# Performance work log

Measured on AMD Instinct MI355X. Metric: run time of the kernel, lower is better.

## Reference

```python
import jax, jax.numpy as jnp
import numpy as np
from jax import lax


def setup_inputs() -> dict:
    key = jax.random.key(0)
    ks = jax.random.split(key, 6)
    B, C, H, W = 8, 128, 64, 64   # C = 2*channel, channel (per-branch) c = 64
    c = C // 2
    return {
        "x_up": jax.random.normal(ks[0], (B, C, H, W), dtype=jnp.float32),
        "x_skip": jax.random.normal(ks[1], (B, C, H, W), dtype=jnp.float32),
        # nn.Linear(c, 2c): weight [out,in], bias [out]
        "kv1_w": jax.random.normal(ks[2], (2 * c, c), dtype=jnp.float32) * 0.05,
        "kv1_b": jnp.zeros((2 * c,), dtype=jnp.float32),
        "kv2_w": jax.random.normal(ks[3], (2 * c, c), dtype=jnp.float32) * 0.05,
        "kv2_b": jnp.zeros((2 * c,), dtype=jnp.float32),
        # Conv2d(2c, 2c, 3, stride 1, pad 1, bias=False), OIHW
        "conv_w": jax.random.normal(ks[4], (C, C, 3, 3), dtype=jnp.float32) * 0.05,
        # BatchNorm2d(2c) in inference form (running stats)
        "bn_gamma": jax.random.normal(ks[5], (C,), dtype=jnp.float32) * 0.1 + 1.0,
        "bn_beta": jnp.zeros((C,), dtype=jnp.float32),
        "bn_mean": jnp.zeros((C,), dtype=jnp.float32),
        "bn_var": jnp.ones((C,), dtype=jnp.float32),
    }


def reference(x_up, x_skip, kv1_w, kv1_b, kv2_w, kv2_b, conv_w,
              bn_gamma, bn_beta, bn_mean, bn_var):
    b, C, h, w = x_up.shape
    c = C // 2
    hw = h * w
    up1, up2 = x_up[:, :c], x_up[:, c:]
    sk1, sk2 = x_skip[:, :c], x_skip[:, c:]

    # ---- spatial attention branch (softmax over last axis, hw x hw) ----
    shortcut1 = up1 + sk1
    u1 = up1.reshape(b, c, hw).transpose(0, 2, 1)   # (b, hw, c)
    s1 = sk1.reshape(b, c, hw).transpose(0, 2, 1)   # (b, hw, c)
    kv = s1 @ kv1_w.T + kv1_b                        # (b, hw, 2c)
    k1, v1 = kv[..., :c], kv[..., c:]
    attn = jax.nn.softmax(jnp.einsum('bnc,bmc->bnm', u1, k1), axis=-1)  # (b, hw, hw)
    sout = jnp.einsum('bnm,bmc->bnc', attn, v1)      # (b, hw, c)
    sout = sout.transpose(0, 2, 1).reshape(b, c, h, w) + shortcut1

    # ---- channel attention branch (softmax over dim=1 of the c x c map) ----
    shortcut2 = up2 + sk2
    u2 = up2.reshape(b, c, hw).transpose(0, 2, 1)    # (b, hw, c)
    s2 = sk2.reshape(b, c, hw).transpose(0, 2, 1)
    kv = s2 @ kv2_w.T + kv2_b                        # (b, hw, 2c)
    k2, v2 = kv[..., :c], kv[..., c:]
    A = jax.nn.softmax(jnp.einsum('bnc,bnd->bcd', u2, k2), axis=1)  # (b, c, c)
    cout = jnp.einsum('bnc,bcd->bnd', v2, A)          # (b, hw, c)
    cout = cout.transpose(0, 2, 1).reshape(b, c, h, w) + shortcut2

    # ---- conv + BN (inference) + ReLU ----
    x = jnp.concatenate([sout, cout], axis=1)         # (b, 2c, h, w)
    y = lax.conv_general_dilated(x, conv_w, (1, 1), 'SAME',
                                 dimension_numbers=('NCHW', 'OIHW', 'NCHW'))
    inv = jax.lax.rsqrt(bn_var + 1e-5)
    y = (y - bn_mean[None, :, None, None]) * (inv * bn_gamma)[None, :, None, None] \
        + bn_beta[None, :, None, None]
    return jax.nn.relu(y)
```

## Files before the change

kernel.cpp:

```cpp
#include <hip/hip_runtime.h>
#include <math.h>

#define HW 4096

typedef __attribute__((ext_vector_type(8))) short bh8;
typedef __attribute__((ext_vector_type(4))) float f32x4;
typedef __attribute__((ext_vector_type(2))) unsigned int u32x2;
typedef unsigned int u32;
typedef unsigned short u16;

__device__ __forceinline__ u16 f2bf(float f) {
  union { float f; u32 u; } v; v.f = f;
  u32 u = v.u;
  return (u16)((u + 0x7FFFu + ((u >> 16) & 1u)) >> 16);
}
__device__ __forceinline__ float bf2f(u16 h) {
  union { u32 u; float f; } v; v.u = ((u32)h) << 16;
  return v.f;
}
__device__ __forceinline__ u32 cvt_pk_bf16(float lo, float hi) {
  u32 r;
  asm("v_cvt_pk_bf16_f32 %0, %1, %2" : "=v"(r) : "v"(lo), "v"(hi));
  return r;
}
__device__ __forceinline__ float fexp2(float x) {
  float r;
  asm("v_exp_f32 %0, %1" : "=v"(r) : "v"(x));
  return r;
}

__global__ __launch_bounds__(256) void kv_proj(
    const float* __restrict__ xs,
    const float* __restrict__ w1, const float* __restrict__ b1,
    const float* __restrict__ w2, const float* __restrict__ b2,
    u32* __restrict__ Knm, u16* __restrict__ Vcm,
    u16* __restrict__ K2t, u16* __restrict__ V2t,
    const float* __restrict__ cw, const float* __restrict__ gamma,
    const float* __restrict__ beta, const float* __restrict__ mean,
    const float* __restrict__ var, u16* __restrict__ Wg,
    float* __restrict__ shb) {
  __shared__ float Ss[64][65];
  __shared__ float Ws[128 * 64];
  __shared__ u32 LtK[64][33];
  const int b = blockIdx.y, n0 = blockIdx.x * 64;
  const int t = threadIdx.x;
  const int lane_n = t & 63, jg = t >> 6;
  const int jbase = jg * 32;
  const float* xsb = xs + (size_t)b * 128 * HW;

  {
    int gid = (blockIdx.y * 64 + blockIdx.x) * 256 + t;
    for (int i = gid; i < 147456; i += 131072) {
      int tap = i >> 14, oc = (i >> 7) & 127, ic = i & 127;
      float sc = gamma[oc] * rsqrtf(var[oc] + 1e-5f);
      Wg[i] = f2bf(cw[((size_t)(oc * 128 + ic)) * 9 + tap] * sc);
    }
    if (gid < 128) {
      float sc = gamma[gid] * rsqrtf(var[gid] + 1e-5f);
      shb[gid] = beta[gid] - mean[gid] * sc;
    }
  }

  for (int br = 0; br < 2; ++br) {
    const float* W = br ? w2 : w1;
    const float* bias = br ? b2 : b1;
    const float* src = xsb + (br ? 64 * HW : 0);
    __syncthreads();
    for (int s = 0; s < 16; ++s) {
      int ch = s * 4 + jg;
      Ss[ch][lane_n] = src[(size_t)ch * HW + n0 + lane_n];
    }
    for (int i = t; i < 128 * 64; i += 256) Ws[i] = W[i];
    __syncthreads();

    float acc[32];
#pragma unroll
    for (int i = 0; i < 32; ++i) acc[i] = bias[jbase + i];
    for (int ch = 0; ch < 64; ++ch) {
      float s = Ss[ch][lane_n];
#pragma unroll
      for (int i = 0; i < 32; ++i) acc[i] = fmaf(Ws[(jbase + i) * 64 + ch], s, acc[i]);
    }

    if (br == 0) {
      if (jg < 2) {
#pragma unroll
        for (int i2 = 0; i2 < 16; ++i2) {
          u32 p = (u32)f2bf(acc[2 * i2]) | ((u32)f2bf(acc[2 * i2 + 1]) << 16);
          LtK[lane_n][jg * 16 + i2] = p;
        }
      } else {
#pragma unroll
        for (int i = 0; i < 32; ++i) {
          int ch = jbase - 64 + i;
          Vcm[((size_t)b * 64 + ch) * HW + n0 + lane_n] = f2bf(acc[i]);
        }
      }
      __syncthreads();
#pragma unroll
      for (int p = 0; p < 8; ++p) {
        int idx = p * 256 + t;
        int n = idx >> 5, cc = idx & 31;
        Knm[((size_t)b * HW + n0 + n) * 32 + cc] = LtK[n][cc];
      }
    } else {
      u16* Kt = K2t + (size_t)b * 64 * HW;
      u16* Vt = V2t + (size_t)b * 64 * HW;
#pragma unroll
      for (int i = 0; i < 32; ++i) {
        int j = jbase + i;
        u16* dst = (j < 64) ? (Kt + (size_t)j * HW) : (Vt + (size_t)(j - 64) * HW);
        dst[n0 + lane_n] = f2bf(acc[i]);
      }
    }
  }
}

__device__ __forceinline__ void attn_step(
    const bh8* kf, const bh8* vf, const bh8 (&qb)[4][2], const bh8 ones,
    f32x4 (&O)[4][4], f32x4 (&Osum)[4]) {
  f32x4 S[2][4];
  __builtin_amdgcn_s_setprio(1);
#pragma unroll
  for (int mt = 0; mt < 2; ++mt)
#pragma unroll
    for (int nt = 0; nt < 4; ++nt) {
      f32x4 a = (f32x4)(0.f);
      a = __builtin_amdgcn_mfma_f32_16x16x32_bf16(kf[mt * 2 + 0], qb[nt][0], a, 0, 0, 0);
      a = __builtin_amdgcn_mfma_f32_16x16x32_bf16(kf[mt * 2 + 1], qb[nt][1], a, 0, 0, 0);
      S[mt][nt] = a;
    }
  __builtin_amdgcn_s_setprio(0);
#pragma unroll
  for (int nt = 0; nt < 4; ++nt) {
    const float c = 17.312340f;
    float e00 = fexp2(S[0][nt][0] - c), e01 = fexp2(S[0][nt][1] - c);
    float e02 = fexp2(S[0][nt][2] - c), e03 = fexp2(S[0][nt][3] - c);
    float e10 = fexp2(S[1][nt][0] - c), e11 = fexp2(S[1][nt][1] - c);
    float e12 = fexp2(S[1][nt][2] - c), e13 = fexp2(S[1][nt][3] - c);
    u32 A = cvt_pk_bf16(e00, e01);
    u32 B = cvt_pk_bf16(e02, e03);
    u32 C = cvt_pk_bf16(e10, e11);
    u32 D = cvt_pk_bf16(e12, e13);
    u32x2 rac = __builtin_amdgcn_permlane32_swap(A, C, 0, 0);
    u32x2 rbd = __builtin_amdgcn_permlane32_swap(B, D, 0, 0);
    u32x2 r02 = __builtin_amdgcn_permlane16_swap(rac.x, rac.y, 0, 0);
    u32x2 r13 = __builtin_amdgcn_permlane16_swap(rbd.x, rbd.y, 0, 0);
    union { u32 u[4]; bh8 v; } pb;
    pb.u[0] = r02.x;
    pb.u[1] = r13.x;
    pb.u[2] = r02.y;
    pb.u[3] = r13.y;
    __builtin_amdgcn_s_setprio(1);
#pragma unroll
    for (int ct = 0; ct < 4; ++ct)
      O[ct][nt] = __builtin_amdgcn_mfma_f32_16x16x32_bf16(vf[ct], pb.v, O[ct][nt], 0, 0, 0);
    Osum[nt] = __builtin_amdgcn_mfma_f32_16x16x32_bf16(ones, pb.v, Osum[nt], 0, 0, 0);
    __builtin_amdgcn_s_setprio(0);
  }
}

#define LOADKV(KB, KF, VF)                                            \
  do {                                                                \
    const int n0_ = (KB) * 128;                                       \
    const u16* kr_ = Kb + (size_t)(n0_ + wb + lq) * 64 + quad * 8;    \
    KF[0] = *(const bh8*)(kr_);                                       \
    KF[1] = *(const bh8*)(kr_ + 32);                                  \
    KF[2] = *(const bh8*)(kr_ + 1024);                                \
    KF[3] = *(const bh8*)(kr_ + 1056);                                \
    const u16* vr_ = Vb + (size_t)lq * HW + n0_ + wb + quad * 8;      \
    VF[0] = *(const bh8*)(vr_);                                       \
    VF[1] = *(const bh8*)(vr_ + 16 * HW);                             \
    VF[2] = *(const bh8*)(vr_ + 32 * HW);                             \
    VF[3] = *(const bh8*)(vr_ + 48 * HW);                             \
  } while (0)

__global__ __launch_bounds__(256, 2) void attn_gram(
    const float* __restrict__ xu, const float* __restrict__ xs,
    const u16* __restrict__ Knm, const u16* __restrict__ Vcm,
    u16* __restrict__ xcat,
    const u16* __restrict__ K2t, float* __restrict__ Mp) {
  __shared__ __align__(16) u16 SMEM[18432];
  const int b = blockIdx.y;
  const int t = threadIdx.x;

  if (blockIdx.x >= 64) {
    float* Us = (float*)SMEM;
    float* Ksm = Us + 64 * 65;
    const int n0 = (blockIdx.x - 64) * 128;
    const int c = t & 63, dg = t >> 6;
    const float* ub = xu + ((size_t)b * 128 + 64) * HW;
    const u16* kb2 = K2t + (size_t)b * 64 * HW;
    float acc[16];
#pragma unroll
    for (int i = 0; i < 16; ++i) acc[i] = 0.f;
    for (int s = 0; s < 2; ++s) {
      int nn = n0 + s * 64;
      __syncthreads();
      for (int r = 0; r < 16; ++r) {
        int row = r * 4 + dg;
        Us[row * 65 + c] = ub[(size_t)row * HW + nn + c];
        Ksm[row * 65 + c] = bf2f(kb2[(size_t)row * HW + nn + c]);
      }
      __syncthreads();
      for (int n = 0; n < 64; ++n) {
        float u = Us[c * 65 + n];
#pragma unroll
        for (int i = 0; i < 16; ++i)
          acc[i] = fmaf(Ksm[(dg * 16 + i) * 65 + n], u, acc[i]);
      }
    }
    float* dst = Mp + ((size_t)(blockIdx.x - 64) * 8 + b) * 4096 + c * 64 + dg * 16;
#pragma unroll
    for (int i = 0; i < 16; ++i) dst[i] = acc[i];
    return;
  }

  const int q0 = blockIdx.x * 64;
  const int wq = t >> 6, lane = t & 63, lq = lane & 15, quad = lane >> 4;
  const int wb = wq * 32;
  const float* xub = xu + (size_t)b * 128 * HW;
  const float* xsb = xs + (size_t)b * 128 * HW;
  const u16* Kb = Knm + (size_t)b * HW * 64;
  const u16* Vb = Vcm + (size_t)b * 64 * HW;

  bh8 qb[4][2];
#pragma unroll
  for (int nt = 0; nt < 4; ++nt)
#pragma unroll
    for (int s = 0; s < 2; ++s)
#pragma unroll
      for (int j = 0; j < 8; ++j) {
        int ch = s * 32 + quad * 8 + j;
        qb[nt][s][j] =
            (short)f2bf(xub[(size_t)ch * HW + q0 + nt * 16 + lq] * 1.44269504f);
      }
  bh8 ones;
#pragma unroll
  for (int j = 0; j < 8; ++j) ones[j] = (short)0x3F80;

  f32x4 O[4][4];
#pragma unroll
  for (int ct = 0; ct < 4; ++ct)
#pragma unroll
    for (int nt = 0; nt < 4; ++nt) O[ct][nt] = (f32x4)(0.f);
  f32x4 Osum[4];
#pragma unroll
  for (int nt = 0; nt < 4; ++nt) Osum[nt] = (f32x4)(0.f);

  bh8 kfa[4], vfa[4], kfb[4], vfb[4];
  LOADKV(0, kfa, vfa);
  for (int kb = 0; kb < 32; kb += 2) {
    LOADKV(kb + 1, kfb, vfb);
    attn_step(kfa, vfa, qb, ones, O, Osum);
    if (kb + 2 < 32) LOADKV(kb + 2, kfa, vfa);
    attn_step(kfb, vfb, qb, ones, O, Osum);
  }

  float* Posc = (float*)SMEM;
  float* Lred = (float*)(SMEM + 17408);
  if (quad == 0) {
#pragma unroll
    for (int nt = 0; nt < 4; ++nt) Lred[(wq * 4 + nt) * 16 + lq] = Osum[nt][0];
  }

  const int q = t & 63, cg = t >> 6;
#pragma unroll
  for (int rh = 0; rh < 2; ++rh) {
    if (rh) __syncthreads();
#pragma unroll
    for (int c2 = 0; c2 < 2; ++c2)
#pragma unroll
      for (int nt = 0; nt < 4; ++nt)
#pragma unroll
        for (int r = 0; r < 4; ++r)
          Posc[(wq * 32 + c2 * 16 + quad * 4 + r) * 68 + nt * 16 + lq] =
              O[rh * 2 + c2][nt][r];
    __syncthreads();
    float li = 0.f;
#pragma unroll
    for (int w2 = 0; w2 < 4; ++w2) li += Lred[w2 * 64 + q];
    float inv = 1.f / li;
    u16 h[8];
#pragma unroll
    for (int i = 0; i < 8; ++i) {
      int chl = cg * 8 + i;
      float s = 0.f;
#pragma unroll
      for (int w2 = 0; w2 < 4; ++w2) s += Posc[(w2 * 32 + chl) * 68 + q];
      int ch = rh * 32 + chl;
      size_t g = (size_t)ch * HW + q0 + q;
      h[i] = f2bf(s * inv + xub[g] + xsb[g]);
    }
    u32 pk[4];
#pragma unroll
    for (int j = 0; j < 4; ++j) pk[j] = (u32)h[2 * j] | ((u32)h[2 * j + 1] << 16);
    u16* ob = xcat + ((size_t)b * HW + q0 + q) * 128 + rh * 32 + cg * 8;
    *(uint4*)ob = make_uint4(pk[0], pk[1], pk[2], pk[3]);
  }
}

__global__ void chan_reduce(const float* __restrict__ Mp, float* __restrict__ M) {
  int idx = blockIdx.x * 256 + threadIdx.x;
  float s = 0.f;
  for (int ch = 0; ch < 32; ++ch) s += Mp[(size_t)ch * 32768 + idx];
  M[idx] = s;
}

__global__ __launch_bounds__(256) void chan_apply(
    const u16* __restrict__ V2t, const float* __restrict__ M,
    const float* __restrict__ xu, const float* __restrict__ xs,
    u16* __restrict__ xcat) {
  __shared__ float Vsm[64][65];
  __shared__ float As[64][65];
  __shared__ float red1[4][64], red2[4][64];
  const int b = blockIdx.y, n0 = blockIdx.x * 64, t = threadIdx.x;
  const int lane = t & 63, dg = t >> 6;
  const u16* Vb = V2t + (size_t)b * 64 * HW;
  for (int s = 0; s < 16; ++s) {
    int c = s * 4 + dg;
    Vsm[lane][c] = bf2f(Vb[(size_t)c * HW + n0 + lane]);
  }
  for (int idx = t; idx < 4096; idx += 256) As[idx >> 6][idx & 63] = M[b * 4096 + idx];
  __syncthreads();
  float mx = -1e30f;
#pragma unroll
  for (int i = 0; i < 16; ++i) mx = fmaxf(mx, As[dg * 16 + i][lane]);
  red1[dg][lane] = mx;
  __syncthreads();
  mx = fmaxf(fmaxf(red1[0][lane], red1[1][lane]), fmaxf(red1[2][lane], red1[3][lane]));
  float se = 0.f;
#pragma unroll
  for (int i = 0; i < 16; ++i) {
    float e = __expf(As[dg * 16 + i][lane] - mx);
    As[dg * 16 + i][lane] = e;
    se += e;
  }
  red2[dg][lane] = se;
  __syncthreads();

  float acc[16];
#pragma unroll
  for (int i = 0; i < 16; ++i) acc[i] = 0.f;
  for (int c = 0; c < 64; ++c) {
    float v = Vsm[lane][c];
#pragma unroll
    for (int i = 0; i < 16; ++i) acc[i] = fmaf(v, As[c][dg * 16 + i], acc[i]);
  }
  const float* xub = xu + ((size_t)b * 128 + 64) * HW;
  const float* xsb = xs + ((size_t)b * 128 + 64) * HW;
  const int n = n0 + lane;
  u16 hv[16];
#pragma unroll
  for (int i = 0; i < 16; ++i) {
    int d = dg * 16 + i;
    float sm = red2[0][d] + red2[1][d] + red2[2][d] + red2[3][d];
    hv[i] = f2bf(acc[i] / sm + xub[(size_t)d * HW + n] + xsb[(size_t)d * HW + n]);
  }
  u32 pk[8];
#pragma unroll
  for (int j = 0; j < 8; ++j) pk[j] = (u32)hv[2 * j] | ((u32)hv[2 * j + 1] << 16);
  u16* ob = xcat + ((size_t)b * HW + n) * 128 + 64 + dg * 16;
  *(uint4*)(ob) = make_uint4(pk[0], pk[1], pk[2], pk[3]);
  *(uint4*)(ob + 8) = make_uint4(pk[4], pk[5], pk[6], pk[7]);
}

__global__ __launch_bounds__(512) void conv_mfma(
    const u16* __restrict__ X, const u16* __restrict__ Wg,
    const float* __restrict__ shb, float* __restrict__ out) {
  __shared__ __align__(16) u16 In[4 * 66 * 136];
  __shared__ __align__(16) u16 Wt[2][128 * 136];
  const int b = blockIdx.y, h0 = blockIdx.x * 2;
  const int t = threadIdx.x;
  const int wq = t >> 6, lane = t & 63, lq = lane & 15, quad = lane >> 4;
  const int nb = (wq & 1) * 64;
  const int mb = (wq >> 1) * 2;
  const u16* Xb = X + (size_t)b * HW * 128;

  if (t < 128) {
    int ih = t >> 5, iwsel = (t >> 4) & 1, ck = t & 15;
    int iw = iwsel ? 65 : 0;
    *(uint4*)&In[(ih * 66 + iw) * 136 + ck * 8] = make_uint4(0, 0, 0, 0);
  }
  for (int ih = 0; ih < 4; ++ih) {
    int h = h0 - 1 + ih;
    bool ok = (h >= 0 && h < 64);
    const u16* src = Xb + (size_t)h * 64 * 128;
#pragma unroll
    for (int p = 0; p < 2; ++p) {
      int idx = p * 512 + t;
      int row = idx >> 4, ck = idx & 15;
      uint4 d = make_uint4(0, 0, 0, 0);
      if (ok) d = *(const uint4*)(src + (size_t)row * 128 + ck * 8);
      *(uint4*)&In[(ih * 66 + 1 + row) * 136 + ck * 8] = d;
    }
  }
  {
    const u16* src = Wg;
#pragma unroll
    for (int p = 0; p < 4; ++p) {
      int idx = p * 512 + t;
      int oc = idx >> 4, ck = idx & 15;
      uint4 d = *(const uint4*)(src + oc * 128 + ck * 8);
      *(uint4*)&Wt[0][oc * 136 + ck * 8] = d;
    }
  }
  __syncthreads();

  f32x4 acc[2][4];
#pragma unroll
  for (int mt = 0; mt < 2; ++mt)
#pragma unroll
    for (int nt = 0; nt < 4; ++nt) acc[mt][nt] = (f32x4)(0.f);

  for (int tap = 0; tap < 9; ++tap) {
    const int cur = tap & 1;
    if (tap < 8) {
      const u16* src = Wg + (size_t)(tap + 1) * 128 * 128;
#pragma unroll
      for (int p = 0; p < 4; ++p) {
        int idx = p * 512 + t;
        int oc = idx >> 4, ck = idx & 15;
        uint4 d = *(const uint4*)(src + oc * 128 + ck * 8);
        *(uint4*)&Wt[cur ^ 1][oc * 136 + ck * 8] = d;
      }
    }
    const int dh = tap / 3, dw = tap - 3 * dh;
    const u16* Wc = &Wt[cur][0];
#pragma unroll
    for (int c = 0; c < 4; ++c) {
      bh8 bf[4];
#pragma unroll
      for (int nt = 0; nt < 4; ++nt)
        bf[nt] = *(const bh8*)&Wc[(nb + nt * 16 + lq) * 136 + c * 32 + quad * 8];
#pragma unroll
      for (int mt = 0; mt < 2; ++mt) {
        int s = (mb + mt) * 16 + lq;
        int ih = (s >> 6) + dh, iw = (s & 63) + dw;
        bh8 af = *(const bh8*)&In[(ih * 66 + iw) * 136 + c * 32 + quad * 8];
#pragma unroll
        for (int nt = 0; nt < 4; ++nt)
          acc[mt][nt] = __builtin_amdgcn_mfma_f32_16x16x32_bf16(af, bf[nt], acc[mt][nt], 0, 0, 0);
      }
    }
    __syncthreads();
  }

  float shv[4];
#pragma unroll
  for (int nt = 0; nt < 4; ++nt) shv[nt] = shb[nb + nt * 16 + lq];
#pragma unroll
  for (int mt = 0; mt < 2; ++mt) {
    int mtile = mb + mt;
    int h = h0 + (mtile >> 2);
    int w0 = ((mtile & 3) * 16) + quad * 4;
#pragma unroll
    for (int nt = 0; nt < 4; ++nt) {
      int oc = nb + nt * 16 + lq;
      float4 v;
      v.x = fmaxf(acc[mt][nt][0] + shv[nt], 0.f);
      v.y = fmaxf(acc[mt][nt][1] + shv[nt], 0.f);
      v.z = fmaxf(acc[mt][nt][2] + shv[nt], 0.f);
      v.w = fmaxf(acc[mt][nt][3] + shv[nt], 0.f);
      *(float4*)&out[((size_t)b * 128 + oc) * HW + h * 64 + w0] = v;
    }
  }
}

extern "C" void kernel_launch(void* const* d_in, const int* in_sizes, int n_in,
                              void* d_out, int out_size, void* d_ws, size_t ws_size,
                              hipStream_t stream) {
  const float* x_up   = (const float*)d_in[0];
  const float* x_skip = (const float*)d_in[1];
  const float* kv1_w  = (const float*)d_in[2];
  const float* kv1_b  = (const float*)d_in[3];
  const float* kv2_w  = (const float*)d_in[4];
  const float* kv2_b  = (const float*)d_in[5];
  const float* conv_w = (const float*)d_in[6];
  const float* bn_g   = (const float*)d_in[7];
  const float* bn_b   = (const float*)d_in[8];
  const float* bn_m   = (const float*)d_in[9];
  const float* bn_v   = (const float*)d_in[10];
  float* out = (float*)d_out;

  char* ws = (char*)d_ws;
  const size_t XCATB_B = (size_t)8 * HW * 128 * 2;
  const size_t KV16_B  = (size_t)8 * 64 * HW * 2;
  size_t off = 0;
  u16*   xcat = (u16*)(ws + off);   off += XCATB_B;
  u16*   K2t  = (u16*)(ws + off);   off += KV16_B;
  u16*   V2t  = (u16*)(ws + off);   off += KV16_B;
  u32*   Knm  = (u32*)(ws + off);   off += KV16_B;
  u16*   Vcm  = (u16*)(ws + off);   off += KV16_B;
  float* Mp   = (float*)(ws + off); off += (size_t)32 * 8 * 4096 * 4;
  float* M    = (float*)(ws + off); off += (size_t)8 * 4096 * 4;
  u16*   Wg   = (u16*)(ws + off);   off += (size_t)9 * 128 * 128 * 2;
  float* shb  = (float*)(ws + off); off += 512;

  kv_proj<<<dim3(64, 8), 256, 0, stream>>>(x_skip, kv1_w, kv1_b, kv2_w, kv2_b,
                                           Knm, Vcm, K2t, V2t,
                                           conv_w, bn_g, bn_b, bn_m, bn_v, Wg, shb);
  attn_gram<<<dim3(96, 8), 256, 0, stream>>>(x_up, x_skip, (const u16*)Knm, Vcm,
                                             xcat, K2t, Mp);
  chan_reduce<<<128, 256, 0, stream>>>(Mp, M);
  chan_apply<<<dim3(64, 8), 256, 0, stream>>>(V2t, M, x_up, x_skip, xcat);
  conv_mfma<<<dim3(32, 8), 512, 0, stream>>>(xcat, Wg, shb, out);
}
```

Baseline: 255.4 us.

## Split attention keys across eight waves per block and halve gram block count

The attention kernel moves from 256 to 512 threads per block, so each block's eight waves split every 256-key chunk and it runs half as many key iterations. Partial outputs and row sums from the eight waves are then reduced through shared memory in four channel passes. The gram blocks cover 256 positions each, which halves their count and the work in chan_reduce. The fixed exponent offset before exp2 is also dropped, since normalisation by the row sum cancels it. The tighter launch bounds (512 threads, 4 blocks) may force register spills, the cross-wave reduction costs more, and the unshifted exp2 can overflow if scores grow large.

```diff
diff --git a/kernel.cpp b/kernel.cpp
--- a/kernel.cpp
+++ b/kernel.cpp
@@ -133,11 +133,10 @@
   __builtin_amdgcn_s_setprio(0);
 #pragma unroll
   for (int nt = 0; nt < 4; ++nt) {
-    const float c = 17.312340f;
-    float e00 = fexp2(S[0][nt][0] - c), e01 = fexp2(S[0][nt][1] - c);
-    float e02 = fexp2(S[0][nt][2] - c), e03 = fexp2(S[0][nt][3] - c);
-    float e10 = fexp2(S[1][nt][0] - c), e11 = fexp2(S[1][nt][1] - c);
-    float e12 = fexp2(S[1][nt][2] - c), e13 = fexp2(S[1][nt][3] - c);
+    float e00 = fexp2(S[0][nt][0]), e01 = fexp2(S[0][nt][1]);
+    float e02 = fexp2(S[0][nt][2]), e03 = fexp2(S[0][nt][3]);
+    float e10 = fexp2(S[1][nt][0]), e11 = fexp2(S[1][nt][1]);
+    float e12 = fexp2(S[1][nt][2]), e13 = fexp2(S[1][nt][3]);
     u32 A = cvt_pk_bf16(e00, e01);
     u32 B = cvt_pk_bf16(e02, e03);
     u32 C = cvt_pk_bf16(e10, e11);
@@ -162,7 +161,7 @@
 
 #define LOADKV(KB, KF, VF)                                            \
   do {                                                                \
-    const int n0_ = (KB) * 128;                                       \
+    const int n0_ = (KB) * 256;                                       \
     const u16* kr_ = Kb + (size_t)(n0_ + wb + lq) * 64 + quad * 8;    \
     KF[0] = *(const bh8*)(kr_);                                       \
     KF[1] = *(const bh8*)(kr_ + 32);                                  \
@@ -175,7 +174,7 @@
     VF[3] = *(const bh8*)(vr_ + 48 * HW);                             \
   } while (0)
 
-__global__ __launch_bounds__(256, 2) void attn_gram(
+__global__ __launch_bounds__(512, 4) void attn_gram(
     const float* __restrict__ xu, const float* __restrict__ xs,
     const u16* __restrict__ Knm, const u16* __restrict__ Vcm,
     u16* __restrict__ xcat,
@@ -187,18 +186,18 @@
   if (blockIdx.x >= 64) {
     float* Us = (float*)SMEM;
     float* Ksm = Us + 64 * 65;
-    const int n0 = (blockIdx.x - 64) * 128;
+    const int n0 = (blockIdx.x - 64) * 256;
     const int c = t & 63, dg = t >> 6;
     const float* ub = xu + ((size_t)b * 128 + 64) * HW;
     const u16* kb2 = K2t + (size_t)b * 64 * HW;
-    float acc[16];
-#pragma unroll
-    for (int i = 0; i < 16; ++i) acc[i] = 0.f;
-    for (int s = 0; s < 2; ++s) {
+    float acc[8];
+#pragma unroll
+    for (int i = 0; i < 8; ++i) acc[i] = 0.f;
+    for (int s = 0; s < 4; ++s) {
       int nn = n0 + s * 64;
       __syncthreads();
-      for (int r = 0; r < 16; ++r) {
-        int row = r * 4 + dg;
+      for (int r = 0; r < 8; ++r) {
+        int row = r * 8 + dg;
         Us[row * 65 + c] = ub[(size_t)row * HW + nn + c];
         Ksm[row * 65 + c] = bf2f(kb2[(size_t)row * HW + nn + c]);
       }
@@ -206,13 +205,13 @@
       for (int n = 0; n < 64; ++n) {
         float u = Us[c * 65 + n];
 #pragma unroll
-        for (int i = 0; i < 16; ++i)
-          acc[i] = fmaf(Ksm[(dg * 16 + i) * 65 + n], u, acc[i]);
-      }
-    }
-    float* dst = Mp + ((size_t)(blockIdx.x - 64) * 8 + b) * 4096 + c * 64 + dg * 16;
-#pragma unroll
-    for (int i = 0; i < 16; ++i) dst[i] = acc[i];
+        for (int i = 0; i < 8; ++i)
+          acc[i] = fmaf(Ksm[(dg * 8 + i) * 65 + n], u, acc[i]);
+      }
+    }
+    float* dst = Mp + ((size_t)(blockIdx.x - 64) * 8 + b) * 4096 + c * 64 + dg * 8;
+#pragma unroll
+    for (int i = 0; i < 8; ++i) dst[i] = acc[i];
     return;
   }
 
@@ -250,10 +249,10 @@
 
   bh8 kfa[4], vfa[4], kfb[4], vfb[4];
   LOADKV(0, kfa, vfa);
-  for (int kb = 0; kb < 32; kb += 2) {
+  for (int kb = 0; kb < 16; kb += 2) {
     LOADKV(kb + 1, kfb, vfb);
     attn_step(kfa, vfa, qb, ones, O, Osum);
-    if (kb + 2 < 32) LOADKV(kb + 2, kfa, vfa);
+    if (kb + 2 < 16) LOADKV(kb + 2, kfa, vfa);
     attn_step(kfb, vfb, qb, ones, O, Osum);
   }
 
@@ -264,46 +263,43 @@
     for (int nt = 0; nt < 4; ++nt) Lred[(wq * 4 + nt) * 16 + lq] = Osum[nt][0];
   }
 
-  const int q = t & 63, cg = t >> 6;
-#pragma unroll
-  for (int rh = 0; rh < 2; ++rh) {
-    if (rh) __syncthreads();
-#pragma unroll
-    for (int c2 = 0; c2 < 2; ++c2)
-#pragma unroll
-      for (int nt = 0; nt < 4; ++nt)
-#pragma unroll
-        for (int r = 0; r < 4; ++r)
-          Posc[(wq * 32 + c2 * 16 + quad * 4 + r) * 68 + nt * 16 + lq] =
-              O[rh * 2 + c2][nt][r];
+  const int q = t >> 3, cs = t & 7;
+  float inv = 0.f;
+#pragma unroll
+  for (int ct = 0; ct < 4; ++ct) {
+    if (ct) __syncthreads();
+#pragma unroll
+    for (int nt = 0; nt < 4; ++nt)
+#pragma unroll
+      for (int r = 0; r < 4; ++r)
+        Posc[(wq * 16 + quad * 4 + r) * 68 + nt * 16 + lq] = O[ct][nt][r];
     __syncthreads();
-    float li = 0.f;
-#pragma unroll
-    for (int w2 = 0; w2 < 4; ++w2) li += Lred[w2 * 64 + q];
-    float inv = 1.f / li;
-    u16 h[8];
-#pragma unroll
-    for (int i = 0; i < 8; ++i) {
-      int chl = cg * 8 + i;
+    if (ct == 0) {
+      float li = 0.f;
+#pragma unroll
+      for (int w2 = 0; w2 < 8; ++w2) li += Lred[w2 * 64 + q];
+      inv = 1.f / li;
+    }
+    u16 h[2];
+#pragma unroll
+    for (int i = 0; i < 2; ++i) {
+      int chl = cs * 2 + i;
       float s = 0.f;
 #pragma unroll
-      for (int w2 = 0; w2 < 4; ++w2) s += Posc[(w2 * 32 + chl) * 68 + q];
-      int ch = rh * 32 + chl;
+      for (int w2 = 0; w2 < 8; ++w2) s += Posc[(w2 * 16 + chl) * 68 + q];
+      int ch = ct * 16 + chl;
       size_t g = (size_t)ch * HW + q0 + q;
       h[i] = f2bf(s * inv + xub[g] + xsb[g]);
     }
-    u32 pk[4];
-#pragma unroll
-    for (int j = 0; j < 4; ++j) pk[j] = (u32)h[2 * j] | ((u32)h[2 * j + 1] << 16);
-    u16* ob = xcat + ((size_t)b * HW + q0 + q) * 128 + rh * 32 + cg * 8;
-    *(uint4*)ob = make_uint4(pk[0], pk[1], pk[2], pk[3]);
+    u32 pk = (u32)h[0] | ((u32)h[1] << 16);
+    *(u32*)(xcat + ((size_t)b * HW + q0 + q) * 128 + ct * 16 + cs * 2) = pk;
   }
 }
 
 __global__ void chan_reduce(const float* __restrict__ Mp, float* __restrict__ M) {
   int idx = blockIdx.x * 256 + threadIdx.x;
   float s = 0.f;
-  for (int ch = 0; ch < 32; ++ch) s += Mp[(size_t)ch * 32768 + idx];
+  for (int ch = 0; ch < 16; ++ch) s += Mp[(size_t)ch * 32768 + idx];
   M[idx] = s;
 }
 
@@ -500,7 +496,7 @@
   kv_proj<<<dim3(64, 8), 256, 0, stream>>>(x_skip, kv1_w, kv1_b, kv2_w, kv2_b,
                                            Knm, Vcm, K2t, V2t,
                                            conv_w, bn_g, bn_b, bn_m, bn_v, Wg, shb);
-  attn_gram<<<dim3(96, 8), 256, 0, stream>>>(x_up, x_skip, (const u16*)Knm, Vcm,
+  attn_gram<<<dim3(80, 8), 512, 0, stream>>>(x_up, x_skip, (const u16*)Knm, Vcm,
                                              xcat, K2t, Mp);
   chan_reduce<<<128, 256, 0, stream>>>(Mp, M);
   chan_apply<<<dim3(64, 8), 256, 0, stream>>>(V2t, M, x_up, x_skip, xcat);
```

New measurement: 655.4 us. +156.6%, slower.

## Halve attention query tile to 32 to double block count, drop exp offset

Applied to the files above, without the earlier changes.

The spatial attention kernel now processes 32 queries per block instead of 64, which doubles the attention grid from 64 to 128 blocks per batch. This should fill more compute units and cut per-thread register use. The epilogue becomes a single LDS pass over all 64 channels instead of two halves. The constant subtraction before exp2 is also removed, which saves an op per element but risks float overflow if the scores grow large. Each block still streams the full K/V set, so K/V reads double in total.

```diff
diff --git a/kernel.cpp b/kernel.cpp
--- a/kernel.cpp
+++ b/kernel.cpp
@@ -117,14 +117,14 @@
 }
 
 __device__ __forceinline__ void attn_step(
-    const bh8* kf, const bh8* vf, const bh8 (&qb)[4][2], const bh8 ones,
-    f32x4 (&O)[4][4], f32x4 (&Osum)[4]) {
-  f32x4 S[2][4];
+    const bh8* kf, const bh8* vf, const bh8 (&qb)[2][2], const bh8 ones,
+    f32x4 (&O)[4][2], f32x4 (&Osum)[2]) {
+  f32x4 S[2][2];
   __builtin_amdgcn_s_setprio(1);
 #pragma unroll
   for (int mt = 0; mt < 2; ++mt)
 #pragma unroll
-    for (int nt = 0; nt < 4; ++nt) {
+    for (int nt = 0; nt < 2; ++nt) {
       f32x4 a = (f32x4)(0.f);
       a = __builtin_amdgcn_mfma_f32_16x16x32_bf16(kf[mt * 2 + 0], qb[nt][0], a, 0, 0, 0);
       a = __builtin_amdgcn_mfma_f32_16x16x32_bf16(kf[mt * 2 + 1], qb[nt][1], a, 0, 0, 0);
@@ -132,12 +132,11 @@
     }
   __builtin_amdgcn_s_setprio(0);
 #pragma unroll
-  for (int nt = 0; nt < 4; ++nt) {
-    const float c = 17.312340f;
-    float e00 = fexp2(S[0][nt][0] - c), e01 = fexp2(S[0][nt][1] - c);
-    float e02 = fexp2(S[0][nt][2] - c), e03 = fexp2(S[0][nt][3] - c);
-    float e10 = fexp2(S[1][nt][0] - c), e11 = fexp2(S[1][nt][1] - c);
-    float e12 = fexp2(S[1][nt][2] - c), e13 = fexp2(S[1][nt][3] - c);
+  for (int nt = 0; nt < 2; ++nt) {
+    float e00 = fexp2(S[0][nt][0]), e01 = fexp2(S[0][nt][1]);
+    float e02 = fexp2(S[0][nt][2]), e03 = fexp2(S[0][nt][3]);
+    float e10 = fexp2(S[1][nt][0]), e11 = fexp2(S[1][nt][1]);
+    float e12 = fexp2(S[1][nt][2]), e13 = fexp2(S[1][nt][3]);
     u32 A = cvt_pk_bf16(e00, e01);
     u32 B = cvt_pk_bf16(e02, e03);
     u32 C = cvt_pk_bf16(e10, e11);
@@ -184,10 +183,10 @@
   const int b = blockIdx.y;
   const int t = threadIdx.x;
 
-  if (blockIdx.x >= 64) {
+  if (blockIdx.x >= 128) {
     float* Us = (float*)SMEM;
     float* Ksm = Us + 64 * 65;
-    const int n0 = (blockIdx.x - 64) * 128;
+    const int n0 = (blockIdx.x - 128) * 128;
     const int c = t & 63, dg = t >> 6;
     const float* ub = xu + ((size_t)b * 128 + 64) * HW;
     const u16* kb2 = K2t + (size_t)b * 64 * HW;
@@ -210,13 +209,13 @@
           acc[i] = fmaf(Ksm[(dg * 16 + i) * 65 + n], u, acc[i]);
       }
     }
-    float* dst = Mp + ((size_t)(blockIdx.x - 64) * 8 + b) * 4096 + c * 64 + dg * 16;
+    float* dst = Mp + ((size_t)(blockIdx.x - 128) * 8 + b) * 4096 + c * 64 + dg * 16;
 #pragma unroll
     for (int i = 0; i < 16; ++i) dst[i] = acc[i];
     return;
   }
 
-  const int q0 = blockIdx.x * 64;
+  const int q0 = blockIdx.x * 32;
   const int wq = t >> 6, lane = t & 63, lq = lane & 15, quad = lane >> 4;
   const int wb = wq * 32;
   const float* xub = xu + (size_t)b * 128 * HW;
@@ -224,9 +223,9 @@
   const u16* Kb = Knm + (size_t)b * HW * 64;
   const u16* Vb = Vcm + (size_t)b * 64 * HW;
 
-  bh8 qb[4][2];
-#pragma unroll
-  for (int nt = 0; nt < 4; ++nt)
+  bh8 qb[2][2];
+#pragma unroll
+  for (int nt = 0; nt < 2; ++nt)
 #pragma unroll
     for (int s = 0; s < 2; ++s)
 #pragma unroll
@@ -239,14 +238,14 @@
 #pragma unroll
   for (int j = 0; j < 8; ++j) ones[j] = (short)0x3F80;
 
-  f32x4 O[4][4];
+  f32x4 O[4][2];
 #pragma unroll
   for (int ct = 0; ct < 4; ++ct)
 #pragma unroll
-    for (int nt = 0; nt < 4; ++nt) O[ct][nt] = (f32x4)(0.f);
-  f32x4 Osum[4];
-#pragma unroll
-  for (int nt = 0; nt < 4; ++nt) Osum[nt] = (f32x4)(0.f);
+    for (int nt = 0; nt < 2; ++nt) O[ct][nt] = (f32x4)(0.f);
+  f32x4 Osum[2];
+#pragma unroll
+  for (int nt = 0; nt < 2; ++nt) Osum[nt] = (f32x4)(0.f);
 
   bh8 kfa[4], vfa[4], kfb[4], vfb[4];
   LOADKV(0, kfa, vfa);
@@ -261,43 +260,35 @@
   float* Lred = (float*)(SMEM + 17408);
   if (quad == 0) {
 #pragma unroll
-    for (int nt = 0; nt < 4; ++nt) Lred[(wq * 4 + nt) * 16 + lq] = Osum[nt][0];
-  }
-
-  const int q = t & 63, cg = t >> 6;
-#pragma unroll
-  for (int rh = 0; rh < 2; ++rh) {
-    if (rh) __syncthreads();
-#pragma unroll
-    for (int c2 = 0; c2 < 2; ++c2)
-#pragma unroll
-      for (int nt = 0; nt < 4; ++nt)
-#pragma unroll
-        for (int r = 0; r < 4; ++r)
-          Posc[(wq * 32 + c2 * 16 + quad * 4 + r) * 68 + nt * 16 + lq] =
-              O[rh * 2 + c2][nt][r];
-    __syncthreads();
-    float li = 0.f;
-#pragma unroll
-    for (int w2 = 0; w2 < 4; ++w2) li += Lred[w2 * 64 + q];
-    float inv = 1.f / li;
-    u16 h[8];
-#pragma unroll
-    for (int i = 0; i < 8; ++i) {
-      int chl = cg * 8 + i;
-      float s = 0.f;
-#pragma unroll
-      for (int w2 = 0; w2 < 4; ++w2) s += Posc[(w2 * 32 + chl) * 68 + q];
-      int ch = rh * 32 + chl;
-      size_t g = (size_t)ch * HW + q0 + q;
-      h[i] = f2bf(s * inv + xub[g] + xsb[g]);
-    }
-    u32 pk[4];
-#pragma unroll
-    for (int j = 0; j < 4; ++j) pk[j] = (u32)h[2 * j] | ((u32)h[2 * j + 1] << 16);
-    u16* ob = xcat + ((size_t)b * HW + q0 + q) * 128 + rh * 32 + cg * 8;
-    *(uint4*)ob = make_uint4(pk[0], pk[1], pk[2], pk[3]);
-  }
+    for (int nt = 0; nt < 2; ++nt) Lred[wq * 32 + nt * 16 + lq] = Osum[nt][0];
+  }
+#pragma unroll
+  for (int ct = 0; ct < 4; ++ct)
+#pragma unroll
+    for (int nt = 0; nt < 2; ++nt)
+#pragma unroll
+      for (int r = 0; r < 4; ++r)
+        Posc[(wq * 64 + ct * 16 + quad * 4 + r) * 34 + nt * 16 + lq] = O[ct][nt][r];
+  __syncthreads();
+
+  const int q = t & 31, cs = t >> 5;
+  float li = Lred[q] + Lred[32 + q] + Lred[64 + q] + Lred[96 + q];
+  float inv = 1.f / li;
+  u16 h[8];
+#pragma unroll
+  for (int i = 0; i < 8; ++i) {
+    int ch = cs * 8 + i;
+    float s = 0.f;
+#pragma unroll
+    for (int w2 = 0; w2 < 4; ++w2) s += Posc[(w2 * 64 + ch) * 34 + q];
+    size_t g = (size_t)ch * HW + q0 + q;
+    h[i] = f2bf(s * inv + xub[g] + xsb[g]);
+  }
+  u32 pk[4];
+#pragma unroll
+  for (int j = 0; j < 4; ++j) pk[j] = (u32)h[2 * j] | ((u32)h[2 * j + 1] << 16);
+  *(uint4*)(xcat + ((size_t)b * HW + q0 + q) * 128 + cs * 8) =
+      make_uint4(pk[0], pk[1], pk[2], pk[3]);
 }
 
 __global__ void chan_reduce(const float* __restrict__ Mp, float* __restrict__ M) {
@@ -500,8 +491,8 @@
   kv_proj<<<dim3(64, 8), 256, 0, stream>>>(x_skip, kv1_w, kv1_b, kv2_w, kv2_b,
                                            Knm, Vcm, K2t, V2t,
                                            conv_w, bn_g, bn_b, bn_m, bn_v, Wg, shb);
-  attn_gram<<<dim3(96, 8), 256, 0, stream>>>(x_up, x_skip, (const u16*)Knm, Vcm,
-                                             xcat, K2t, Mp);
+  attn_gram<<<dim3(160, 8), 256, 0, stream>>>(x_up, x_skip, (const u16*)Knm, Vcm,
+                                              xcat, K2t, Mp);
   chan_reduce<<<128, 256, 0, stream>>>(Mp, M);
   chan_apply<<<dim3(64, 8), 256, 0, stream>>>(V2t, M, x_up, x_skip, xcat);
   conv_mfma<<<dim3(32, 8), 512, 0, stream>>>(xcat, Wg, shb, out);
```

Result: slower. 330.2 us (+29.3%).
